# Optimization experiments

Hardware: AMD Instinct MI355X
Metric: run time of the kernel (lower is better)

Reference implementation:

```python
import jax, jax.numpy as jnp
import numpy as np

SIGMA = 1.0
RADIUS = 4  # skimage.filters.gaussian: truncate=4.0 -> radius=int(4.0*1.0+0.5)=4 (9 taps)
NBINS = 256  # skimage.filters.threshold_otsu default


def _gauss_kernel(dtype):
    x = jnp.arange(-RADIUS, RADIUS + 1, dtype=dtype)
    k = jnp.exp(-0.5 * (x / SIGMA) ** 2)
    return k / k.sum()


def _blur(img):
    # img: [B, H, W]; separable Gaussian, 'nearest' (edge) boundary like scipy/skimage.
    k = _gauss_kernel(img.dtype)
    p = jnp.pad(img, ((0, 0), (RADIUS, RADIUS), (0, 0)), mode='edge')
    out = jax.lax.conv_general_dilated(p[:, None], k.reshape(1, 1, 2 * RADIUS + 1, 1),
                                       (1, 1), 'VALID')[:, 0]
    p = jnp.pad(out, ((0, 0), (0, 0), (RADIUS, RADIUS)), mode='edge')
    out = jax.lax.conv_general_dilated(p[:, None], k.reshape(1, 1, 1, 2 * RADIUS + 1),
                                       (1, 1), 'VALID')[:, 0]
    return out


def _otsu(img):
    # img: [H, W] -> scalar Otsu threshold (256-bin histogram over [min, max]).
    lo, hi = img.min(), img.max()
    width = (hi - lo) / NBINS
    idx = jnp.clip(jnp.floor((img - lo) / jnp.maximum(width, 1e-12)).astype(jnp.int32),
                   0, NBINS - 1)
    counts = jnp.zeros(NBINS, img.dtype).at[idx.ravel()].add(1.0)
    centers = lo + (jnp.arange(NBINS, dtype=img.dtype) + 0.5) * width
    w1 = jnp.cumsum(counts)                      # class-0 weight
    w2 = jnp.cumsum(counts[::-1])[::-1]          # class-1 weight
    cs = jnp.cumsum(counts * centers)
    rcs = jnp.cumsum((counts * centers)[::-1])[::-1]
    m1 = cs / jnp.maximum(w1, 1e-12)
    m2 = rcs / jnp.maximum(w2, 1e-12)
    var12 = w1[:-1] * w2[1:] * (m1[:-1] - m2[1:]) ** 2
    return centers[jnp.argmax(var12)]


def reference(x):
    # x: [B, 4, H, W]; channel 0 = thermal (normalized mean=std=0.5), last 3 = RGB.
    thermal = jnp.clip(x[:, 0] * 0.5 + 0.5, 0.0, 1.0)          # denormalize [B,H,W]
    blurred = _blur(thermal)
    t = jax.vmap(_otsu)(blurred)                               # [B]
    mask = jnp.where(blurred > t[:, None, None], 1.0, blurred)  # soft alpha mask
    rgb = x[:, -3:]                                            # [B,3,H,W]
    alpha = mask[:, None]                                      # [B,1,H,W]
    # skimage rgba2rgb with white background: clip(alpha*rgb + (1-alpha)*1)
    return jnp.clip(alpha * rgb + (1.0 - alpha), 0.0, 1.0)


def setup_inputs() -> dict:
    key = jax.random.key(0)
    x = jax.random.normal(key, (32, 4, 512, 512), dtype=jnp.float32)
    return {"x": x}
```

## Files before the change

kernel.cpp:

```cpp
#include <hip/hip_runtime.h>
#include <math.h>

#pragma clang fp contract(off)

struct GaussW { float w[9]; };

__global__ __launch_bounds__(256) void blur_kernel(const float* __restrict__ x,
                                                   float* __restrict__ blurred,
                                                   float* __restrict__ pmin,
                                                   float* __restrict__ pmax,
                                                   unsigned* __restrict__ hist, GaussW gw) {
    #pragma clang fp contract(off)
    __shared__ float s_in[72][72];
    __shared__ float s_vb[64][72];
    const int tid = threadIdx.x;
    const int b = blockIdx.z;
    const int r0 = blockIdx.y * 64, c0 = blockIdx.x * 64;
    if (blockIdx.x == 0 && blockIdx.y == 0) hist[b * 256 + tid] = 0u;
    const float* img0 = x + (size_t)b * 4 * 262144;

    for (int i = tid; i < 72 * 72; i += 256) {
        int r = i / 72, c = i - r * 72;
        int gr = min(max(r0 + r - 4, 0), 511);
        int gc = min(max(c0 + c - 4, 0), 511);
        float v = img0[gr * 512 + gc];
        s_in[r][c] = fminf(fmaxf(v * 0.5f + 0.5f, 0.0f), 1.0f);
    }
    __syncthreads();
    for (int i = tid; i < 64 * 72; i += 256) {
        int r = i / 72, c = i - r * 72;
        float q0 = s_in[r + 0][c] * gw.w[0];
        float q1 = s_in[r + 1][c] * gw.w[1];
        float q2 = s_in[r + 2][c] * gw.w[2];
        float q3 = s_in[r + 3][c] * gw.w[3];
        float q4 = s_in[r + 4][c] * gw.w[4];
        float q5 = s_in[r + 5][c] * gw.w[5];
        float q6 = s_in[r + 6][c] * gw.w[6];
        float q7 = s_in[r + 7][c] * gw.w[7];
        float q8 = s_in[r + 8][c] * gw.w[8];
        float acc = ((q0 + q1) + (q2 + q3)) + ((q4 + q5) + (q6 + q7));
        acc = acc + q8;
        s_vb[r][c] = acc;
    }
    __syncthreads();
    float lmin = 1e30f, lmax = -1e30f;
    float* bimg = blurred + (size_t)b * 262144;
    for (int i = tid; i < 64 * 64; i += 256) {
        int r = i >> 6, c = i & 63;
        float q0 = s_vb[r][c + 0] * gw.w[0];
        float q1 = s_vb[r][c + 1] * gw.w[1];
        float q2 = s_vb[r][c + 2] * gw.w[2];
        float q3 = s_vb[r][c + 3] * gw.w[3];
        float q4 = s_vb[r][c + 4] * gw.w[4];
        float q5 = s_vb[r][c + 5] * gw.w[5];
        float q6 = s_vb[r][c + 6] * gw.w[6];
        float q7 = s_vb[r][c + 7] * gw.w[7];
        float q8 = s_vb[r][c + 8] * gw.w[8];
        float acc = ((q0 + q1) + (q2 + q3)) + ((q4 + q5) + (q6 + q7));
        acc = acc + q8;
        bimg[(r0 + r) * 512 + (c0 + c)] = acc;
        lmin = fminf(lmin, acc);
        lmax = fmaxf(lmax, acc);
    }
    for (int off = 32; off >= 1; off >>= 1) {
        lmin = fminf(lmin, __shfl_down(lmin, off));
        lmax = fmaxf(lmax, __shfl_down(lmax, off));
    }
    __shared__ float smin[4], smax[4];
    int wave = tid >> 6, lane = tid & 63;
    if (lane == 0) { smin[wave] = lmin; smax[wave] = lmax; }
    __syncthreads();
    if (tid == 0) {
        float mn = fminf(fminf(smin[0], smin[1]), fminf(smin[2], smin[3]));
        float mx = fmaxf(fmaxf(smax[0], smax[1]), fmaxf(smax[2], smax[3]));
        int bid = blockIdx.y * 8 + blockIdx.x;
        pmin[b * 64 + bid] = mn;
        pmax[b * 64 + bid] = mx;
    }
}

__global__ __launch_bounds__(256) void hist_kernel(const float* __restrict__ blurred,
                                                   const float* __restrict__ pmin,
                                                   const float* __restrict__ pmax,
                                                   unsigned* __restrict__ hist) {
    #pragma clang fp contract(off)
    const int b = blockIdx.y;
    __shared__ unsigned sh[256];
    __shared__ float s_lo, s_hi;
    sh[threadIdx.x] = 0u;
    int wv = threadIdx.x >> 6, ln = threadIdx.x & 63;
    if (wv == 0) {
        float v = pmin[b * 64 + ln];
        for (int off = 32; off >= 1; off >>= 1) v = fminf(v, __shfl_down(v, off));
        if (ln == 0) s_lo = v;
    } else if (wv == 1) {
        float v = pmax[b * 64 + ln];
        for (int off = 32; off >= 1; off >>= 1) v = fmaxf(v, __shfl_down(v, off));
        if (ln == 0) s_hi = v;
    }
    __syncthreads();
    const float lo = s_lo, hi = s_hi;
    const float width = (hi - lo) * 0.00390625f;
    const float denom = fmaxf(width, 1e-12f);
    const float4* img = (const float4*)(blurred + (size_t)b * 262144);
    for (int i = blockIdx.x * 256 + threadIdx.x; i < 65536; i += gridDim.x * 256) {
        float4 v = img[i];
        int i0 = min(max((int)floorf((v.x - lo) / denom), 0), 255);
        int i1 = min(max((int)floorf((v.y - lo) / denom), 0), 255);
        int i2 = min(max((int)floorf((v.z - lo) / denom), 0), 255);
        int i3 = min(max((int)floorf((v.w - lo) / denom), 0), 255);
        atomicAdd(&sh[i0], 1u);
        atomicAdd(&sh[i1], 1u);
        atomicAdd(&sh[i2], 1u);
        atomicAdd(&sh[i3], 1u);
    }
    __syncthreads();
    unsigned cnt = sh[threadIdx.x];
    if (cnt) atomicAdd(&hist[b * 256 + threadIdx.x], cnt);
}

__global__ __launch_bounds__(256) void otsu_kernel(const unsigned* __restrict__ hist,
                                                   const float* __restrict__ pmin,
                                                   const float* __restrict__ pmax,
                                                   float* __restrict__ t) {
    #pragma clang fp contract(off)
    __shared__ float counts[256], centers[256], w1[256], w2[256], cs[256], rcs[256];
    __shared__ float s_lo, s_hi;
    const int b = blockIdx.x, tid = threadIdx.x;
    const int wv = tid >> 6, ln = tid & 63;
    if (wv == 0) {
        float v = pmin[b * 64 + ln];
        for (int off = 32; off >= 1; off >>= 1) v = fminf(v, __shfl_down(v, off));
        if (ln == 0) s_lo = v;
    } else if (wv == 1) {
        float v = pmax[b * 64 + ln];
        for (int off = 32; off >= 1; off >>= 1) v = fmaxf(v, __shfl_down(v, off));
        if (ln == 0) s_hi = v;
    }
    __syncthreads();
    const float lo = s_lo, hi = s_hi;
    const float width = (hi - lo) * 0.00390625f;
    counts[tid] = (float)hist[b * 256 + tid];
    centers[tid] = lo + ((float)tid + 0.5f) * width;
    __syncthreads();
    if (ln == 0) {
        if (wv == 0) {
            float a = 0.f;
            for (int i0 = 0; i0 < 256; i0 += 8) {
                float c0 = counts[i0+0], c1 = counts[i0+1], c2 = counts[i0+2], c3 = counts[i0+3];
                float c4 = counts[i0+4], c5 = counts[i0+5], c6 = counts[i0+6], c7 = counts[i0+7];
                a = a + c0; w1[i0+0] = a; a = a + c1; w1[i0+1] = a;
                a = a + c2; w1[i0+2] = a; a = a + c3; w1[i0+3] = a;
                a = a + c4; w1[i0+4] = a; a = a + c5; w1[i0+5] = a;
                a = a + c6; w1[i0+6] = a; a = a + c7; w1[i0+7] = a;
            }
        } else if (wv == 1) {
            float a = 0.f;
            for (int i0 = 255; i0 >= 7; i0 -= 8) {
                float c0 = counts[i0-0], c1 = counts[i0-1], c2 = counts[i0-2], c3 = counts[i0-3];
                float c4 = counts[i0-4], c5 = counts[i0-5], c6 = counts[i0-6], c7 = counts[i0-7];
                a = a + c0; w2[i0-0] = a; a = a + c1; w2[i0-1] = a;
                a = a + c2; w2[i0-2] = a; a = a + c3; w2[i0-3] = a;
                a = a + c4; w2[i0-4] = a; a = a + c5; w2[i0-5] = a;
                a = a + c6; w2[i0-6] = a; a = a + c7; w2[i0-7] = a;
            }
        } else if (wv == 2) {
            float a = 0.f;
            for (int i0 = 0; i0 < 256; i0 += 8) {
                float q0 = counts[i0+0] * centers[i0+0], q1 = counts[i0+1] * centers[i0+1];
                float q2 = counts[i0+2] * centers[i0+2], q3 = counts[i0+3] * centers[i0+3];
                float q4 = counts[i0+4] * centers[i0+4], q5 = counts[i0+5] * centers[i0+5];
                float q6 = counts[i0+6] * centers[i0+6], q7 = counts[i0+7] * centers[i0+7];
                a = a + q0; cs[i0+0] = a; a = a + q1; cs[i0+1] = a;
                a = a + q2; cs[i0+2] = a; a = a + q3; cs[i0+3] = a;
                a = a + q4; cs[i0+4] = a; a = a + q5; cs[i0+5] = a;
                a = a + q6; cs[i0+6] = a; a = a + q7; cs[i0+7] = a;
            }
        } else {
            float a = 0.f;
            for (int i0 = 255; i0 >= 7; i0 -= 8) {
                float q0 = counts[i0-0] * centers[i0-0], q1 = counts[i0-1] * centers[i0-1];
                float q2 = counts[i0-2] * centers[i0-2], q3 = counts[i0-3] * centers[i0-3];
                float q4 = counts[i0-4] * centers[i0-4], q5 = counts[i0-5] * centers[i0-5];
                float q6 = counts[i0-6] * centers[i0-6], q7 = counts[i0-7] * centers[i0-7];
                a = a + q0; rcs[i0-0] = a; a = a + q1; rcs[i0-1] = a;
                a = a + q2; rcs[i0-2] = a; a = a + q3; rcs[i0-3] = a;
                a = a + q4; rcs[i0-4] = a; a = a + q5; rcs[i0-5] = a;
                a = a + q6; rcs[i0-6] = a; a = a + q7; rcs[i0-7] = a;
            }
        }
    }
    __syncthreads();
    if (wv == 0) {
        float best = -1e30f; int bi = 0x7fffffff;
#pragma unroll
        for (int k = 0; k < 4; ++k) {
            int i = ln + 64 * k;
            if (i < 255) {
                float m1 = cs[i] / fmaxf(w1[i], 1e-12f);
                float m2 = rcs[i + 1] / fmaxf(w2[i + 1], 1e-12f);
                float d = m1 - m2;
                float v = (w1[i] * w2[i + 1]) * (d * d);
                if (v > best) { best = v; bi = i; }
            }
        }
        for (int off = 32; off >= 1; off >>= 1) {
            float ov = __shfl_down(best, off);
            int   oi = __shfl_down(bi, off);
            if (ov > best || (ov == best && oi < bi)) { best = ov; bi = oi; }
        }
        if (ln == 0) t[b] = centers[bi];
    }
}

__global__ __launch_bounds__(256) void final_kernel(const float* __restrict__ x,
                                                    const float* __restrict__ blurred,
                                                    const float* __restrict__ tarr,
                                                    float* __restrict__ out, int total4) {
    #pragma clang fp contract(off)
    int i = blockIdx.x * 256 + threadIdx.x;
    if (i >= total4) return;
    int b = i >> 16;
    int p = i & 65535;
    float tb = tarr[b];
    float4 bl = ((const float4*)(blurred + (size_t)b * 262144))[p];
    float4 m;
    m.x = (bl.x > tb) ? 1.0f : bl.x;
    m.y = (bl.y > tb) ? 1.0f : bl.y;
    m.z = (bl.z > tb) ? 1.0f : bl.z;
    m.w = (bl.w > tb) ? 1.0f : bl.w;
    const float4* xim = (const float4*)(x + (size_t)b * 4 * 262144);
    float4* oim = (float4*)(out + (size_t)b * 3 * 262144);
#pragma unroll
    for (int c = 0; c < 3; ++c) {
        float4 rgb = xim[(size_t)(c + 1) * 65536 + p];
        float4 o;
        o.x = fminf(fmaxf(m.x * rgb.x + (1.0f - m.x), 0.f), 1.f);
        o.y = fminf(fmaxf(m.y * rgb.y + (1.0f - m.y), 0.f), 1.f);
        o.z = fminf(fmaxf(m.z * rgb.z + (1.0f - m.z), 0.f), 1.f);
        o.w = fminf(fmaxf(m.w * rgb.w + (1.0f - m.w), 0.f), 1.f);
        oim[(size_t)c * 65536 + p] = o;
    }
}

extern "C" void kernel_launch(void* const* d_in, const int* in_sizes, int n_in,
                              void* d_out, int out_size, void* d_ws, size_t ws_size,
                              hipStream_t stream) {
    const float* x = (const float*)d_in[0];
    float* out = (float*)d_out;
    const int nimg = in_sizes[0] / (4 * 262144);

    float* blurred = (float*)d_ws;
    unsigned* hist = (unsigned*)(blurred + (size_t)nimg * 262144);
    float* pmin = (float*)(hist + (size_t)nimg * 256);
    float* pmax = pmin + (size_t)nimg * 64;
    float* t = pmax + (size_t)nimg * 64;

    GaussW gw;
    float kk[9];
    for (int i = 0; i < 9; ++i) {
        double d = (double)(i - 4);
        kk[i] = (float)exp(-0.5 * d * d);
    }
    float s = ((kk[0] + kk[1]) + (kk[2] + kk[3])) + ((kk[4] + kk[5]) + (kk[6] + kk[7]));
    s = s + kk[8];
    for (int i = 0; i < 9; ++i) gw.w[i] = kk[i] / s;

    dim3 bgrid(8, 8, nimg);
    blur_kernel<<<bgrid, 256, 0, stream>>>(x, blurred, pmin, pmax, hist, gw);
    dim3 hgrid(16, nimg);
    hist_kernel<<<hgrid, 256, 0, stream>>>(blurred, pmin, pmax, hist);
    otsu_kernel<<<nimg, 256, 0, stream>>>(hist, pmin, pmax, t);
    int total4 = nimg * 65536;
    final_kernel<<<(total4 + 255) / 256, 256, 0, stream>>>(x, blurred, t, out, total4);
}
```

Before: 257.8 us.

## Register-block blur passes and replicate shared histogram to cut atomic contention

The vertical blur pass now computes four output rows per thread from twelve loaded values. The horizontal pass computes four adjacent outputs from three float4 shared-memory loads and writes a float4 to global memory. This cuts redundant LDS reads and makes the global stores wider. The histogram kernel keeps eight interleaved copies of each bin in shared memory to reduce atomic contention, at the cost of more LDS use and a final reduction over the copies.

```diff
diff --git a/kernel.cpp b/kernel.cpp
--- a/kernel.cpp
+++ b/kernel.cpp
@@ -27,40 +27,76 @@
         s_in[r][c] = fminf(fmaxf(v * 0.5f + 0.5f, 0.0f), 1.0f);
     }
     __syncthreads();
-    for (int i = tid; i < 64 * 72; i += 256) {
-        int r = i / 72, c = i - r * 72;
-        float q0 = s_in[r + 0][c] * gw.w[0];
-        float q1 = s_in[r + 1][c] * gw.w[1];
-        float q2 = s_in[r + 2][c] * gw.w[2];
-        float q3 = s_in[r + 3][c] * gw.w[3];
-        float q4 = s_in[r + 4][c] * gw.w[4];
-        float q5 = s_in[r + 5][c] * gw.w[5];
-        float q6 = s_in[r + 6][c] * gw.w[6];
-        float q7 = s_in[r + 7][c] * gw.w[7];
-        float q8 = s_in[r + 8][c] * gw.w[8];
-        float acc = ((q0 + q1) + (q2 + q3)) + ((q4 + q5) + (q6 + q7));
-        acc = acc + q8;
-        s_vb[r][c] = acc;
+    for (int i = tid; i < 1152; i += 256) {
+        int sr = (i / 72) * 4, c = i % 72;
+        float t0 = s_in[sr + 0][c], t1 = s_in[sr + 1][c], t2 = s_in[sr + 2][c];
+        float t3 = s_in[sr + 3][c], t4 = s_in[sr + 4][c], t5 = s_in[sr + 5][c];
+        float t6 = s_in[sr + 6][c], t7 = s_in[sr + 7][c], t8 = s_in[sr + 8][c];
+        float t9 = s_in[sr + 9][c], t10 = s_in[sr + 10][c], t11 = s_in[sr + 11][c];
+        {
+            float q0 = t0 * gw.w[0], q1 = t1 * gw.w[1], q2 = t2 * gw.w[2], q3 = t3 * gw.w[3];
+            float q4 = t4 * gw.w[4], q5 = t5 * gw.w[5], q6 = t6 * gw.w[6], q7 = t7 * gw.w[7];
+            float acc = ((q0 + q1) + (q2 + q3)) + ((q4 + q5) + (q6 + q7));
+            s_vb[sr + 0][c] = acc + t8 * gw.w[8];
+        }
+        {
+            float q0 = t1 * gw.w[0], q1 = t2 * gw.w[1], q2 = t3 * gw.w[2], q3 = t4 * gw.w[3];
+            float q4 = t5 * gw.w[4], q5 = t6 * gw.w[5], q6 = t7 * gw.w[6], q7 = t8 * gw.w[7];
+            float acc = ((q0 + q1) + (q2 + q3)) + ((q4 + q5) + (q6 + q7));
+            s_vb[sr + 1][c] = acc + t9 * gw.w[8];
+        }
+        {
+            float q0 = t2 * gw.w[0], q1 = t3 * gw.w[1], q2 = t4 * gw.w[2], q3 = t5 * gw.w[3];
+            float q4 = t6 * gw.w[4], q5 = t7 * gw.w[5], q6 = t8 * gw.w[6], q7 = t9 * gw.w[7];
+            float acc = ((q0 + q1) + (q2 + q3)) + ((q4 + q5) + (q6 + q7));
+            s_vb[sr + 2][c] = acc + t10 * gw.w[8];
+        }
+        {
+            float q0 = t3 * gw.w[0], q1 = t4 * gw.w[1], q2 = t5 * gw.w[2], q3 = t6 * gw.w[3];
+            float q4 = t7 * gw.w[4], q5 = t8 * gw.w[5], q6 = t9 * gw.w[6], q7 = t10 * gw.w[7];
+            float acc = ((q0 + q1) + (q2 + q3)) + ((q4 + q5) + (q6 + q7));
+            s_vb[sr + 3][c] = acc + t11 * gw.w[8];
+        }
     }
     __syncthreads();
     float lmin = 1e30f, lmax = -1e30f;
     float* bimg = blurred + (size_t)b * 262144;
-    for (int i = tid; i < 64 * 64; i += 256) {
-        int r = i >> 6, c = i & 63;
-        float q0 = s_vb[r][c + 0] * gw.w[0];
-        float q1 = s_vb[r][c + 1] * gw.w[1];
-        float q2 = s_vb[r][c + 2] * gw.w[2];
-        float q3 = s_vb[r][c + 3] * gw.w[3];
-        float q4 = s_vb[r][c + 4] * gw.w[4];
-        float q5 = s_vb[r][c + 5] * gw.w[5];
-        float q6 = s_vb[r][c + 6] * gw.w[6];
-        float q7 = s_vb[r][c + 7] * gw.w[7];
-        float q8 = s_vb[r][c + 8] * gw.w[8];
-        float acc = ((q0 + q1) + (q2 + q3)) + ((q4 + q5) + (q6 + q7));
-        acc = acc + q8;
-        bimg[(r0 + r) * 512 + (c0 + c)] = acc;
-        lmin = fminf(lmin, acc);
-        lmax = fmaxf(lmax, acc);
+    for (int i = tid; i < 1024; i += 256) {
+        int r = i >> 4, cc = (i & 15) * 4;
+        float4 va = *(const float4*)&s_vb[r][cc];
+        float4 vb = *(const float4*)&s_vb[r][cc + 4];
+        float4 vc = *(const float4*)&s_vb[r][cc + 8];
+        float t0 = va.x, t1 = va.y, t2 = va.z, t3 = va.w;
+        float t4 = vb.x, t5 = vb.y, t6 = vb.z, t7 = vb.w;
+        float t8 = vc.x, t9 = vc.y, t10 = vc.z, t11 = vc.w;
+        float4 o;
+        {
+            float q0 = t0 * gw.w[0], q1 = t1 * gw.w[1], q2 = t2 * gw.w[2], q3 = t3 * gw.w[3];
+            float q4 = t4 * gw.w[4], q5 = t5 * gw.w[5], q6 = t6 * gw.w[6], q7 = t7 * gw.w[7];
+            float acc = ((q0 + q1) + (q2 + q3)) + ((q4 + q5) + (q6 + q7));
+            o.x = acc + t8 * gw.w[8];
+        }
+        {
+            float q0 = t1 * gw.w[0], q1 = t2 * gw.w[1], q2 = t3 * gw.w[2], q3 = t4 * gw.w[3];
+            float q4 = t5 * gw.w[4], q5 = t6 * gw.w[5], q6 = t7 * gw.w[6], q7 = t8 * gw.w[7];
+            float acc = ((q0 + q1) + (q2 + q3)) + ((q4 + q5) + (q6 + q7));
+            o.y = acc + t9 * gw.w[8];
+        }
+        {
+            float q0 = t2 * gw.w[0], q1 = t3 * gw.w[1], q2 = t4 * gw.w[2], q3 = t5 * gw.w[3];
+            float q4 = t6 * gw.w[4], q5 = t7 * gw.w[5], q6 = t8 * gw.w[6], q7 = t9 * gw.w[7];
+            float acc = ((q0 + q1) + (q2 + q3)) + ((q4 + q5) + (q6 + q7));
+            o.z = acc + t10 * gw.w[8];
+        }
+        {
+            float q0 = t3 * gw.w[0], q1 = t4 * gw.w[1], q2 = t5 * gw.w[2], q3 = t6 * gw.w[3];
+            float q4 = t7 * gw.w[4], q5 = t8 * gw.w[5], q6 = t9 * gw.w[6], q7 = t10 * gw.w[7];
+            float acc = ((q0 + q1) + (q2 + q3)) + ((q4 + q5) + (q6 + q7));
+            o.w = acc + t11 * gw.w[8];
+        }
+        *(float4*)&bimg[(size_t)(r0 + r) * 512 + (c0 + cc)] = o;
+        lmin = fminf(fminf(fminf(lmin, o.x), fminf(o.y, o.z)), o.w);
+        lmax = fmaxf(fmaxf(fmaxf(lmax, o.x), fmaxf(o.y, o.z)), o.w);
     }
     for (int off = 32; off >= 1; off >>= 1) {
         lmin = fminf(lmin, __shfl_down(lmin, off));
@@ -85,9 +121,9 @@
                                                    unsigned* __restrict__ hist) {
     #pragma clang fp contract(off)
     const int b = blockIdx.y;
-    __shared__ unsigned sh[256];
+    __shared__ unsigned sh[2048];
     __shared__ float s_lo, s_hi;
-    sh[threadIdx.x] = 0u;
+    for (int i = threadIdx.x; i < 2048; i += 256) sh[i] = 0u;
     int wv = threadIdx.x >> 6, ln = threadIdx.x & 63;
     if (wv == 0) {
         float v = pmin[b * 64 + ln];
@@ -102,6 +138,7 @@
     const float lo = s_lo, hi = s_hi;
     const float width = (hi - lo) * 0.00390625f;
     const float denom = fmaxf(width, 1e-12f);
+    const int copy = threadIdx.x & 7;
     const float4* img = (const float4*)(blurred + (size_t)b * 262144);
     for (int i = blockIdx.x * 256 + threadIdx.x; i < 65536; i += gridDim.x * 256) {
         float4 v = img[i];
@@ -109,13 +146,16 @@
         int i1 = min(max((int)floorf((v.y - lo) / denom), 0), 255);
         int i2 = min(max((int)floorf((v.z - lo) / denom), 0), 255);
         int i3 = min(max((int)floorf((v.w - lo) / denom), 0), 255);
-        atomicAdd(&sh[i0], 1u);
-        atomicAdd(&sh[i1], 1u);
-        atomicAdd(&sh[i2], 1u);
-        atomicAdd(&sh[i3], 1u);
-    }
-    __syncthreads();
-    unsigned cnt = sh[threadIdx.x];
+        atomicAdd(&sh[i0 * 8 + copy], 1u);
+        atomicAdd(&sh[i1 * 8 + copy], 1u);
+        atomicAdd(&sh[i2 * 8 + copy], 1u);
+        atomicAdd(&sh[i3 * 8 + copy], 1u);
+    }
+    __syncthreads();
+    unsigned cnt = 0;
+    int base = threadIdx.x * 8;
+#pragma unroll
+    for (int k = 0; k < 8; ++k) cnt += sh[base + k];
     if (cnt) atomicAdd(&hist[b * 256 + threadIdx.x], cnt);
 }
 
```

After: 254.0 us. No clear change (-1.5%).
